# Kernel tuning notes

Measured on AMD Instinct MI355X. Metric: run time of the kernel, lower is better.

## Reference

```python
import jax, jax.numpy as jnp
import numpy as np

N_NODES = 100000
N_EDGES = 400000
N_REL = 3
N_LAYERS = 2
D = 128          # input feature dim == hidden_dim so weights stack cleanly
N_CLASSES = 2


def setup_inputs() -> dict:
    key = jax.random.key(0)
    ks = jax.random.split(key, 7)
    x = jax.random.normal(ks[0], (N_NODES, D), dtype=jnp.float32)
    edge_index = jax.random.randint(ks[1], (N_REL, 2, N_EDGES), 0, N_NODES, dtype=jnp.int32)
    # SAGEConv params per (layer, relation): neighbor weight, root weight, bias
    Wn = jax.random.normal(ks[2], (N_LAYERS, N_REL, D, D), dtype=jnp.float32) * (1.0 / np.sqrt(D))
    Wr = jax.random.normal(ks[3], (N_LAYERS, N_REL, D, D), dtype=jnp.float32) * (1.0 / np.sqrt(D))
    b = jax.random.normal(ks[4], (N_LAYERS, N_REL, D), dtype=jnp.float32) * 0.02
    Wc = jax.random.normal(ks[5], (D, N_CLASSES), dtype=jnp.float32) * (1.0 / np.sqrt(D))
    bc = jax.random.normal(ks[6], (N_CLASSES,), dtype=jnp.float32) * 0.02
    return {"x": x, "edge_index": edge_index, "Wn": Wn, "Wr": Wr, "b": b, "Wc": Wc, "bc": bc}


def _mean_agg(h, ei, n_nodes):
    # gather source features, scatter-mean into destination nodes
    src, dst = ei[0], ei[1]
    s = jax.ops.segment_sum(h[src], dst, num_segments=n_nodes)          # [N, D]
    cnt = jax.ops.segment_sum(jnp.ones((ei.shape[1],), h.dtype), dst, num_segments=n_nodes)
    return s / jnp.maximum(cnt, 1.0)[:, None]


def reference(x, edge_index, Wn, Wr, b, Wc, bc):
    n = x.shape[0]
    h = x
    L, R = Wn.shape[0], Wn.shape[1]
    for l in range(L):
        out = jnp.zeros((n, Wn.shape[-1]), h.dtype)
        for r in range(R):
            # SAGEConv: lin_l(mean neighbors) + lin_r(root) + bias; HeteroConv sums relations
            agg = _mean_agg(h, edge_index[r], n)
            out = out + agg @ Wn[l, r] + h @ Wr[l, r] + b[l, r]
        h = jax.nn.relu(out) if l < L - 1 else out  # dropout is eval-mode identity
    return h @ Wc + bc
```

## Files before the change

### kernel.cpp

```cpp
#include <hip/hip_runtime.h>

#define NN 100000
#define NE 400000
#define NR 3
#define DD 128
#define NROWS (NR * NN)
#define NEDGES (NR * NE)
#define SCAN_BLOCKS ((NROWS + 1023) / 1024)

typedef float f32x4 __attribute__((ext_vector_type(4)));
typedef __bf16 bf16x8 __attribute__((ext_vector_type(8)));

__device__ __forceinline__ unsigned short f2bf(float f) {
    unsigned int u = __float_as_uint(f);
    u += 0x7fff + ((u >> 16) & 1);
    return (unsigned short)(u >> 16);
}

__device__ __forceinline__ void gload16(const void* g, void* l) {
    __builtin_amdgcn_global_load_lds(
        (const __attribute__((address_space(1))) void*)g,
        (__attribute__((address_space(3))) void*)l, 16, 0, 0);
}

#define NB_CVT 6250
#define NB_WT 512
#define NB_ZERO 586
__global__ __launch_bounds__(256) void prep_all(const float* __restrict__ x,
                                                const float* __restrict__ Wn,
                                                const float* __restrict__ Wr,
                                                const float* __restrict__ b,
                                                unsigned short* __restrict__ xb,
                                                unsigned short* __restrict__ Wt2,
                                                float* __restrict__ bias,
                                                unsigned int* __restrict__ zbase) {
    int bid = blockIdx.x;
    int tid = threadIdx.x;
    if (bid < NB_CVT) {
        int i = bid * 256 + tid;
        const float4* xf = reinterpret_cast<const float4*>(x + (size_t)i * 8);
        float4 a = xf[0], bv = xf[1];
        uint4 o;
        o.x = (unsigned)f2bf(a.x) | ((unsigned)f2bf(a.y) << 16);
        o.y = (unsigned)f2bf(a.z) | ((unsigned)f2bf(a.w) << 16);
        o.z = (unsigned)f2bf(bv.x) | ((unsigned)f2bf(bv.y) << 16);
        o.w = (unsigned)f2bf(bv.z) | ((unsigned)f2bf(bv.w) << 16);
        reinterpret_cast<uint4*>(xb)[i] = o;
    } else if (bid < NB_CVT + NB_WT) {
        int t = (bid - NB_CVT) * 256 + tid;
        int l = t >> 16;
        int rem = t & 65535;
        int n512 = rem >> 7;
        int kk = rem & 127;
        int rk = n512 >> 7, n = n512 & 127;
        float v;
        if (rk < 3) {
            v = Wn[(((size_t)l * 3 + rk) * 128 + kk) * 128 + n];
        } else {
            const float* WrL = Wr + (size_t)l * 3 * 128 * 128;
            v = WrL[kk * 128 + n] + WrL[128 * 128 + kk * 128 + n] + WrL[2 * 128 * 128 + kk * 128 + n];
        }
        Wt2[t] = f2bf(v);
    } else if (bid == NB_CVT + NB_WT) {
        int l = tid >> 7, n = tid & 127;
        bias[tid] = b[l * 384 + n] + b[l * 384 + 128 + n] + b[l * 384 + 256 + n];
    } else {
        int i = (bid - NB_CVT - NB_WT - 1) * 256 + tid;
        if (i < 150000) reinterpret_cast<uint4*>(zbase)[i] = make_uint4(0, 0, 0, 0);
    }
}

__global__ __launch_bounds__(256) void csr_count(const int* __restrict__ ei,
                                                 int* __restrict__ cnt) {
    int t = blockIdx.x * 256 + threadIdx.x;
    if (t >= NEDGES) return;
    int r = t / NE;
    int e = t - r * NE;
    int dst = ei[(r * 2 + 1) * NE + e];
    atomicAdd(&cnt[r * NN + dst], 1);
}

__global__ __launch_bounds__(256) void scan1(const int* __restrict__ cnt,
                                             int* __restrict__ row_start,
                                             int* __restrict__ bsum) {
    __shared__ int sh[256];
    int b0 = blockIdx.x * 1024;
    int t = threadIdx.x;
    int v[4];
    int s = 0;
    #pragma unroll
    for (int j = 0; j < 4; ++j) {
        int idx = b0 + t * 4 + j;
        v[j] = (idx < NROWS) ? cnt[idx] : 0;
        s += v[j];
    }
    sh[t] = s;
    __syncthreads();
    for (int off = 1; off < 256; off <<= 1) {
        int val = (t >= off) ? sh[t - off] : 0;
        __syncthreads();
        sh[t] += val;
        __syncthreads();
    }
    int excl = (t == 0) ? 0 : sh[t - 1];
    if (t == 255) bsum[blockIdx.x] = sh[255];
    #pragma unroll
    for (int j = 0; j < 4; ++j) {
        int idx = b0 + t * 4 + j;
        if (idx < NROWS) { row_start[idx] = excl; excl += v[j]; }
    }
}

__global__ __launch_bounds__(512) void scan2(int* __restrict__ bsum, int nb) {
    __shared__ int sh[512];
    int t = threadIdx.x;
    sh[t] = (t < nb) ? bsum[t] : 0;
    __syncthreads();
    for (int off = 1; off < 512; off <<= 1) {
        int val = (t >= off) ? sh[t - off] : 0;
        __syncthreads();
        sh[t] += val;
        __syncthreads();
    }
    int excl = (t == 0) ? 0 : sh[t - 1];
    if (t < nb) bsum[t] = excl;
}

__global__ __launch_bounds__(256) void csr_fill(const int* __restrict__ ei,
                                                const int* __restrict__ row_start,
                                                const int* __restrict__ bsum,
                                                int* __restrict__ cursor,
                                                int* __restrict__ bucket) {
    int t = blockIdx.x * 256 + threadIdx.x;
    if (t >= NEDGES) return;
    int r = t / NE;
    int e = t - r * NE;
    int src = ei[(r * 2 + 0) * NE + e];
    int dst = ei[(r * 2 + 1) * NE + e];
    int i = r * NN + dst;
    int pos = row_start[i] + bsum[i >> 10] + atomicAdd(&cursor[i], 1);
    bucket[pos] = src << 10;
}

__global__ __launch_bounds__(256) void gemm_y(
    const unsigned short* __restrict__ Ab,
    const unsigned short* __restrict__ WtL,
    unsigned short* __restrict__ Yb)
{
    __shared__ __align__(16) unsigned short As[2 * 128 * 32];
    __shared__ __align__(16) unsigned short Bs[2 * 128 * 32];
    const int t = threadIdx.x;
    const int w = t >> 6, lane = t & 63;
    const int bid = blockIdx.x;
    const int p = bid & 3;
    const int m0 = (bid >> 2) * 128;
    const unsigned short* WtP = WtL + p * 128 * 128;
    const int wr = w >> 1, wcol = w & 1;
    const int fr = lane & 15;
    const int fq = lane >> 4;
    const int gsw = (((lane & 3) ^ ((lane >> 2) & 3) ^ ((lane >> 4) & 3))) * 8;
    const int rsw = (fq ^ ((fr ^ (fr >> 2)) & 3)) * 8;
    f32x4 acc[4][4] = {};

    auto stage = [&](int s, int buf) {
        const int k0 = s * 32;
        #pragma unroll
        for (int i = 0; i < 2; ++i) {
            int row = i * 64 + w * 16 + (lane >> 2);
            int grow = m0 + row;
            if (grow > NN - 1) grow = NN - 1;
            const unsigned short* gA = Ab + (size_t)grow * DD + k0 + gsw;
            gload16(gA, (char*)As + buf * 8192 + i * 4096 + w * 1024);
            const unsigned short* gB = WtP + (size_t)row * 128 + k0 + gsw;
            gload16(gB, (char*)Bs + buf * 8192 + i * 4096 + w * 1024);
        }
    };

    stage(0, 0);
    #pragma unroll
    for (int s = 0; s < 4; ++s) {
        const int cur = s & 1;
        __syncthreads();
        if (s + 1 < 4) stage(s + 1, cur ^ 1);
        const unsigned short* As_c = As + cur * 4096;
        const unsigned short* Bs_c = Bs + cur * 4096;
        bf16x8 af[4], bfr[4];
        #pragma unroll
        for (int m = 0; m < 4; ++m)
            af[m] = *reinterpret_cast<const bf16x8*>(As_c + (wr * 64 + m * 16 + fr) * 32 + rsw);
        #pragma unroll
        for (int n = 0; n < 4; ++n)
            bfr[n] = *reinterpret_cast<const bf16x8*>(Bs_c + (wcol * 64 + n * 16 + fr) * 32 + rsw);
        #pragma unroll
        for (int m = 0; m < 4; ++m)
            #pragma unroll
            for (int n = 0; n < 4; ++n)
                acc[m][n] = __builtin_amdgcn_mfma_f32_16x16x32_bf16(af[m], bfr[n], acc[m][n], 0, 0, 0);
    }

    #pragma unroll
    for (int n = 0; n < 4; ++n) {
        int col = p * 128 + wcol * 64 + n * 16 + fr;
        #pragma unroll
        for (int m = 0; m < 4; ++m) {
            int rbase = m0 + wr * 64 + m * 16 + fq * 4;
            #pragma unroll
            for (int j = 0; j < 4; ++j) {
                int row = rbase + j;
                if (row < NN) Yb[(size_t)row * 512 + col] = f2bf(acc[m][n][j]);
            }
        }
    }
}

template <int FINAL>
__global__ __launch_bounds__(256) void gather_fused(
    const unsigned short* __restrict__ Yb,
    const int* __restrict__ bucket,
    const int* __restrict__ row_start,
    const int* __restrict__ bsum,
    const int* __restrict__ cnt,
    const float* __restrict__ biasL,
    const float* __restrict__ Wc,
    const float* __restrict__ bc,
    unsigned short* __restrict__ hout,
    float* __restrict__ out)
{
    int wid = (blockIdx.x * 256 + threadIdx.x) >> 6;
    int lane = threadIdx.x & 63;
    if (wid >= NN) return;
    const char* Yc = (const char*)Yb;
    const unsigned int lo = lane * 4u;
    unsigned int rootv = *(const unsigned int*)(Yc + (size_t)wid * 1024u + 768u + lo);
    float t0 = __uint_as_float(rootv << 16);
    float t1 = __uint_as_float(rootv & 0xffff0000u);
    #pragma unroll
    for (int r = 0; r < 3; ++r) {
        int id = r * NN + wid;
        int base = row_start[id] + bsum[id >> 10];
        int deg = cnt[id];
        unsigned int rb = r * 256u + lo;
        float a0 = 0.f, a1 = 0.f, b0 = 0.f, b1 = 0.f;
        float c0 = 0.f, c1 = 0.f, d0 = 0.f, d1 = 0.f;
        int e = 0;
        for (; e + 4 <= deg; e += 4) {
            unsigned int o0 = (unsigned)bucket[base + e + 0] + rb;
            unsigned int o1 = (unsigned)bucket[base + e + 1] + rb;
            unsigned int o2 = (unsigned)bucket[base + e + 2] + rb;
            unsigned int o3 = (unsigned)bucket[base + e + 3] + rb;
            unsigned int v0 = *(const unsigned int*)(Yc + o0);
            unsigned int v1 = *(const unsigned int*)(Yc + o1);
            unsigned int v2 = *(const unsigned int*)(Yc + o2);
            unsigned int v3 = *(const unsigned int*)(Yc + o3);
            a0 += __uint_as_float(v0 << 16); a1 += __uint_as_float(v0 & 0xffff0000u);
            b0 += __uint_as_float(v1 << 16); b1 += __uint_as_float(v1 & 0xffff0000u);
            c0 += __uint_as_float(v2 << 16); c1 += __uint_as_float(v2 & 0xffff0000u);
            d0 += __uint_as_float(v3 << 16); d1 += __uint_as_float(v3 & 0xffff0000u);
        }
        for (; e < deg; ++e) {
            unsigned int o0 = (unsigned)bucket[base + e] + rb;
            unsigned int v0 = *(const unsigned int*)(Yc + o0);
            a0 += __uint_as_float(v0 << 16); a1 += __uint_as_float(v0 & 0xffff0000u);
        }
        float s0 = (a0 + b0) + (c0 + d0);
        float s1 = (a1 + b1) + (c1 + d1);
        float iv = (deg > 0) ? (1.0f / (float)deg) : 0.0f;
        t0 = fmaf(s0, iv, t0);
        t1 = fmaf(s1, iv, t1);
    }
    float2 bb = reinterpret_cast<const float2*>(biasL)[lane];
    t0 += bb.x;
    t1 += bb.y;
    if (!FINAL) {
        t0 = fmaxf(t0, 0.f);
        t1 = fmaxf(t1, 0.f);
        unsigned int o = (unsigned)f2bf(t0) | ((unsigned)f2bf(t1) << 16);
        reinterpret_cast<unsigned int*>(hout)[wid * 64 + lane] = o;
    } else {
        float4 w4 = reinterpret_cast<const float4*>(Wc)[lane];
        float p0 = t0 * w4.x + t1 * w4.z;
        float p1 = t0 * w4.y + t1 * w4.w;
        #pragma unroll
        for (int off = 1; off < 64; off <<= 1) {
            p0 += __shfl_xor(p0, off);
            p1 += __shfl_xor(p1, off);
        }
        if (lane == 0) {
            out[(size_t)wid * 2 + 0] = p0 + bc[0];
            out[(size_t)wid * 2 + 1] = p1 + bc[1];
        }
    }
}

extern "C" void kernel_launch(void* const* d_in, const int* in_sizes, int n_in,
                              void* d_out, int out_size, void* d_ws, size_t ws_size,
                              hipStream_t stream) {
    const float* x  = (const float*)d_in[0];
    const int*   ei = (const int*)d_in[1];
    const float* Wn = (const float*)d_in[2];
    const float* Wr = (const float*)d_in[3];
    const float* b  = (const float*)d_in[4];
    const float* Wc = (const float*)d_in[5];
    const float* bc = (const float*)d_in[6];
    float* out = (float*)d_out;

    char* p = (char*)d_ws;
    unsigned short* Yb  = (unsigned short*)p;  p += (size_t)NN * 512 * 2;
    unsigned short* xb  = (unsigned short*)p;  p += (size_t)NN * DD * 2;
    unsigned short* h1b = (unsigned short*)p;  p += (size_t)NN * DD * 2;
    unsigned short* Wt2 = (unsigned short*)p;  p += (size_t)2 * 4 * 128 * 128 * 2;
    float* bias         = (float*)p;           p += 2 * 128 * 4;
    int* bucket         = (int*)p;             p += (size_t)NEDGES * 4;
    int* row_start      = (int*)p;             p += (size_t)NROWS * 4;
    int* bsum           = (int*)p;             p += 512 * 4;
    int* cnt            = (int*)p;             p += (size_t)NROWS * 4;
    int* cursor         = (int*)p;             p += (size_t)NROWS * 4;

    prep_all<<<NB_CVT + NB_WT + 1 + NB_ZERO, 256, 0, stream>>>(
        x, Wn, Wr, b, xb, Wt2, bias, (unsigned int*)cnt);

    csr_count<<<(NEDGES + 255) / 256, 256, 0, stream>>>(ei, cnt);
    scan1<<<SCAN_BLOCKS, 256, 0, stream>>>(cnt, row_start, bsum);
    scan2<<<1, 512, 0, stream>>>(bsum, SCAN_BLOCKS);
    csr_fill<<<(NEDGES + 255) / 256, 256, 0, stream>>>(ei, row_start, bsum, cursor, bucket);

    const int gemmBlocks = ((NN + 127) / 128) * 4;
    const int gatherBlocks = NN * 64 / 256;

    gemm_y<<<gemmBlocks, 256, 0, stream>>>(xb, Wt2, Yb);
    gather_fused<0><<<gatherBlocks, 256, 0, stream>>>(Yb, bucket, row_start, bsum, cnt,
                                                      bias, nullptr, nullptr, h1b, nullptr);

    gemm_y<<<gemmBlocks, 256, 0, stream>>>(h1b, Wt2 + (size_t)4 * 128 * 128, Yb);
    gather_fused<1><<<gatherBlocks, 256, 0, stream>>>(Yb, bucket, row_start, bsum, cnt,
                                                      bias + 128, Wc, bc, nullptr, out);
}
```

Before: 485.4 us.

## Interleave CSR rows by node and gather 16-byte rows with 4 edges per wave

The CSR rows are reindexed from relation-major to node-major (dst*3+r), so the three relations of a node sit next to each other and are walked as one edge list. Each bucket entry now holds the relation offset and the precomputed 1/deg scale, so per-relation degree lookups and divides leave the gather loop. The gather splits the wave into 4 groups of 16 lanes, each loading one edge's 256-byte row as uint4, and combines the groups with shuffles at the end. This is meant to raise memory-level parallelism and use wider loads. The cost is a bucket array twice as large and extra cross-lane reductions.

```diff
diff --git a/kernel.cpp b/kernel.cpp
--- a/kernel.cpp
+++ b/kernel.cpp
@@ -16,6 +16,8 @@
     u += 0x7fff + ((u >> 16) & 1);
     return (unsigned short)(u >> 16);
 }
+__device__ __forceinline__ float bflo(unsigned int u) { return __uint_as_float(u << 16); }
+__device__ __forceinline__ float bfhi(unsigned int u) { return __uint_as_float(u & 0xffff0000u); }
 
 __device__ __forceinline__ void gload16(const void* g, void* l) {
     __builtin_amdgcn_global_load_lds(
@@ -77,7 +79,7 @@
     int r = t / NE;
     int e = t - r * NE;
     int dst = ei[(r * 2 + 1) * NE + e];
-    atomicAdd(&cnt[r * NN + dst], 1);
+    atomicAdd(&cnt[dst * 3 + r], 1);
 }
 
 __global__ __launch_bounds__(256) void scan1(const int* __restrict__ cnt,
@@ -129,17 +131,19 @@
 __global__ __launch_bounds__(256) void csr_fill(const int* __restrict__ ei,
                                                 const int* __restrict__ row_start,
                                                 const int* __restrict__ bsum,
+                                                const int* __restrict__ cnt,
                                                 int* __restrict__ cursor,
-                                                int* __restrict__ bucket) {
+                                                int2* __restrict__ bucket2) {
     int t = blockIdx.x * 256 + threadIdx.x;
     if (t >= NEDGES) return;
     int r = t / NE;
     int e = t - r * NE;
     int src = ei[(r * 2 + 0) * NE + e];
     int dst = ei[(r * 2 + 1) * NE + e];
-    int i = r * NN + dst;
+    int i = dst * 3 + r;
     int pos = row_start[i] + bsum[i >> 10] + atomicAdd(&cursor[i], 1);
-    bucket[pos] = src << 10;
+    float sc = 1.0f / (float)cnt[i];
+    bucket2[pos] = make_int2((src << 10) | (r << 8), __float_as_int(sc));
 }
 
 __global__ __launch_bounds__(256) void gemm_y(
@@ -216,7 +220,7 @@
 template <int FINAL>
 __global__ __launch_bounds__(256) void gather_fused(
     const unsigned short* __restrict__ Yb,
-    const int* __restrict__ bucket,
+    const int2* __restrict__ bucket2,
     const int* __restrict__ row_start,
     const int* __restrict__ bsum,
     const int* __restrict__ cnt,
@@ -229,59 +233,78 @@
     int wid = (blockIdx.x * 256 + threadIdx.x) >> 6;
     int lane = threadIdx.x & 63;
     if (wid >= NN) return;
+    const int g = lane >> 4;
+    const int q = lane & 15;
+    const unsigned int qoff = q * 16u;
     const char* Yc = (const char*)Yb;
-    const unsigned int lo = lane * 4u;
-    unsigned int rootv = *(const unsigned int*)(Yc + (size_t)wid * 1024u + 768u + lo);
-    float t0 = __uint_as_float(rootv << 16);
-    float t1 = __uint_as_float(rootv & 0xffff0000u);
-    #pragma unroll
-    for (int r = 0; r < 3; ++r) {
-        int id = r * NN + wid;
-        int base = row_start[id] + bsum[id >> 10];
-        int deg = cnt[id];
-        unsigned int rb = r * 256u + lo;
-        float a0 = 0.f, a1 = 0.f, b0 = 0.f, b1 = 0.f;
-        float c0 = 0.f, c1 = 0.f, d0 = 0.f, d1 = 0.f;
-        int e = 0;
-        for (; e + 4 <= deg; e += 4) {
-            unsigned int o0 = (unsigned)bucket[base + e + 0] + rb;
-            unsigned int o1 = (unsigned)bucket[base + e + 1] + rb;
-            unsigned int o2 = (unsigned)bucket[base + e + 2] + rb;
-            unsigned int o3 = (unsigned)bucket[base + e + 3] + rb;
-            unsigned int v0 = *(const unsigned int*)(Yc + o0);
-            unsigned int v1 = *(const unsigned int*)(Yc + o1);
-            unsigned int v2 = *(const unsigned int*)(Yc + o2);
-            unsigned int v3 = *(const unsigned int*)(Yc + o3);
-            a0 += __uint_as_float(v0 << 16); a1 += __uint_as_float(v0 & 0xffff0000u);
-            b0 += __uint_as_float(v1 << 16); b1 += __uint_as_float(v1 & 0xffff0000u);
-            c0 += __uint_as_float(v2 << 16); c1 += __uint_as_float(v2 & 0xffff0000u);
-            d0 += __uint_as_float(v3 << 16); d1 += __uint_as_float(v3 & 0xffff0000u);
-        }
-        for (; e < deg; ++e) {
-            unsigned int o0 = (unsigned)bucket[base + e] + rb;
-            unsigned int v0 = *(const unsigned int*)(Yc + o0);
-            a0 += __uint_as_float(v0 << 16); a1 += __uint_as_float(v0 & 0xffff0000u);
-        }
-        float s0 = (a0 + b0) + (c0 + d0);
-        float s1 = (a1 + b1) + (c1 + d1);
-        float iv = (deg > 0) ? (1.0f / (float)deg) : 0.0f;
-        t0 = fmaf(s0, iv, t0);
-        t1 = fmaf(s1, iv, t1);
-    }
-    float2 bb = reinterpret_cast<const float2*>(biasL)[lane];
-    t0 += bb.x;
-    t1 += bb.y;
+    const int r3 = wid * 3;
+    const int base = row_start[r3] + bsum[r3 >> 10];
+    const int degT = cnt[r3] + cnt[r3 + 1] + cnt[r3 + 2];
+
+    float acc[8] = {};
+    int e = 0;
+    for (; e + 8 <= degT; e += 8) {
+        int2 ma = bucket2[base + e + g];
+        int2 mb = bucket2[base + e + 4 + g];
+        uint4 va = *(const uint4*)(Yc + (unsigned)ma.x + qoff);
+        uint4 vb = *(const uint4*)(Yc + (unsigned)mb.x + qoff);
+        float sa = __int_as_float(ma.y);
+        float sb = __int_as_float(mb.y);
+        acc[0] = fmaf(bflo(va.x), sa, acc[0]); acc[1] = fmaf(bfhi(va.x), sa, acc[1]);
+        acc[2] = fmaf(bflo(va.y), sa, acc[2]); acc[3] = fmaf(bfhi(va.y), sa, acc[3]);
+        acc[4] = fmaf(bflo(va.z), sa, acc[4]); acc[5] = fmaf(bfhi(va.z), sa, acc[5]);
+        acc[6] = fmaf(bflo(va.w), sa, acc[6]); acc[7] = fmaf(bfhi(va.w), sa, acc[7]);
+        acc[0] = fmaf(bflo(vb.x), sb, acc[0]); acc[1] = fmaf(bfhi(vb.x), sb, acc[1]);
+        acc[2] = fmaf(bflo(vb.y), sb, acc[2]); acc[3] = fmaf(bfhi(vb.y), sb, acc[3]);
+        acc[4] = fmaf(bflo(vb.z), sb, acc[4]); acc[5] = fmaf(bfhi(vb.z), sb, acc[5]);
+        acc[6] = fmaf(bflo(vb.w), sb, acc[6]); acc[7] = fmaf(bfhi(vb.w), sb, acc[7]);
+    }
+    for (; e < degT; e += 4) {
+        if (e + g < degT) {
+            int2 m = bucket2[base + e + g];
+            uint4 v = *(const uint4*)(Yc + (unsigned)m.x + qoff);
+            float s = __int_as_float(m.y);
+            acc[0] = fmaf(bflo(v.x), s, acc[0]); acc[1] = fmaf(bfhi(v.x), s, acc[1]);
+            acc[2] = fmaf(bflo(v.y), s, acc[2]); acc[3] = fmaf(bfhi(v.y), s, acc[3]);
+            acc[4] = fmaf(bflo(v.z), s, acc[4]); acc[5] = fmaf(bfhi(v.z), s, acc[5]);
+            acc[6] = fmaf(bflo(v.w), s, acc[6]); acc[7] = fmaf(bfhi(v.w), s, acc[7]);
+        }
+    }
+    #pragma unroll
+    for (int j = 0; j < 8; ++j) {
+        acc[j] += __shfl_xor(acc[j], 16);
+        acc[j] += __shfl_xor(acc[j], 32);
+    }
+    uint4 rv = *(const uint4*)(Yc + (size_t)wid * 1024u + 768u + qoff);
+    acc[0] += bflo(rv.x); acc[1] += bfhi(rv.x);
+    acc[2] += bflo(rv.y); acc[3] += bfhi(rv.y);
+    acc[4] += bflo(rv.z); acc[5] += bfhi(rv.z);
+    acc[6] += bflo(rv.w); acc[7] += bfhi(rv.w);
+    float4 b0 = *(const float4*)(biasL + q * 8);
+    float4 b1 = *(const float4*)(biasL + q * 8 + 4);
+    acc[0] += b0.x; acc[1] += b0.y; acc[2] += b0.z; acc[3] += b0.w;
+    acc[4] += b1.x; acc[5] += b1.y; acc[6] += b1.z; acc[7] += b1.w;
+
     if (!FINAL) {
-        t0 = fmaxf(t0, 0.f);
-        t1 = fmaxf(t1, 0.f);
-        unsigned int o = (unsigned)f2bf(t0) | ((unsigned)f2bf(t1) << 16);
-        reinterpret_cast<unsigned int*>(hout)[wid * 64 + lane] = o;
+        if (g == 0) {
+            uint4 o;
+            o.x = (unsigned)f2bf(fmaxf(acc[0], 0.f)) | ((unsigned)f2bf(fmaxf(acc[1], 0.f)) << 16);
+            o.y = (unsigned)f2bf(fmaxf(acc[2], 0.f)) | ((unsigned)f2bf(fmaxf(acc[3], 0.f)) << 16);
+            o.z = (unsigned)f2bf(fmaxf(acc[4], 0.f)) | ((unsigned)f2bf(fmaxf(acc[5], 0.f)) << 16);
+            o.w = (unsigned)f2bf(fmaxf(acc[6], 0.f)) | ((unsigned)f2bf(fmaxf(acc[7], 0.f)) << 16);
+            *reinterpret_cast<uint4*>(hout + (size_t)wid * DD + q * 8) = o;
+        }
     } else {
-        float4 w4 = reinterpret_cast<const float4*>(Wc)[lane];
-        float p0 = t0 * w4.x + t1 * w4.z;
-        float p1 = t0 * w4.y + t1 * w4.w;
-        #pragma unroll
-        for (int off = 1; off < 64; off <<= 1) {
+        float4 w0 = *(const float4*)(Wc + q * 16);
+        float4 w1 = *(const float4*)(Wc + q * 16 + 4);
+        float4 w2 = *(const float4*)(Wc + q * 16 + 8);
+        float4 w3 = *(const float4*)(Wc + q * 16 + 12);
+        float p0 = acc[0] * w0.x + acc[1] * w0.z + acc[2] * w1.x + acc[3] * w1.z +
+                   acc[4] * w2.x + acc[5] * w2.z + acc[6] * w3.x + acc[7] * w3.z;
+        float p1 = acc[0] * w0.y + acc[1] * w0.w + acc[2] * w1.y + acc[3] * w1.w +
+                   acc[4] * w2.y + acc[5] * w2.w + acc[6] * w3.y + acc[7] * w3.w;
+        #pragma unroll
+        for (int off = 1; off < 16; off <<= 1) {
             p0 += __shfl_xor(p0, off);
             p1 += __shfl_xor(p1, off);
         }
@@ -310,7 +333,7 @@
     unsigned short* h1b = (unsigned short*)p;  p += (size_t)NN * DD * 2;
     unsigned short* Wt2 = (unsigned short*)p;  p += (size_t)2 * 4 * 128 * 128 * 2;
     float* bias         = (float*)p;           p += 2 * 128 * 4;
-    int* bucket         = (int*)p;             p += (size_t)NEDGES * 4;
+    int2* bucket2       = (int2*)p;            p += (size_t)NEDGES * 8;
     int* row_start      = (int*)p;             p += (size_t)NROWS * 4;
     int* bsum           = (int*)p;             p += 512 * 4;
     int* cnt            = (int*)p;             p += (size_t)NROWS * 4;
@@ -322,16 +345,16 @@
     csr_count<<<(NEDGES + 255) / 256, 256, 0, stream>>>(ei, cnt);
     scan1<<<SCAN_BLOCKS, 256, 0, stream>>>(cnt, row_start, bsum);
     scan2<<<1, 512, 0, stream>>>(bsum, SCAN_BLOCKS);
-    csr_fill<<<(NEDGES + 255) / 256, 256, 0, stream>>>(ei, row_start, bsum, cursor, bucket);
+    csr_fill<<<(NEDGES + 255) / 256, 256, 0, stream>>>(ei, row_start, bsum, cnt, cursor, bucket2);
 
     const int gemmBlocks = ((NN + 127) / 128) * 4;
     const int gatherBlocks = NN * 64 / 256;
 
     gemm_y<<<gemmBlocks, 256, 0, stream>>>(xb, Wt2, Yb);
-    gather_fused<0><<<gatherBlocks, 256, 0, stream>>>(Yb, bucket, row_start, bsum, cnt,
+    gather_fused<0><<<gatherBlocks, 256, 0, stream>>>(Yb, bucket2, row_start, bsum, cnt,
                                                       bias, nullptr, nullptr, h1b, nullptr);
 
     gemm_y<<<gemmBlocks, 256, 0, stream>>>(h1b, Wt2 + (size_t)4 * 128 * 128, Yb);
-    gather_fused<1><<<gatherBlocks, 256, 0, stream>>>(Yb, bucket, row_start, bsum, cnt,
+    gather_fused<1><<<gatherBlocks, 256, 0, stream>>>(Yb, bucket2, row_start, bsum, cnt,
                                                       bias + 128, Wc, bc, nullptr, out);
 }
```

New measurement: 441.4 us. 1.1x faster.
